# Kernel optimization log

Measured on AMD Instinct MI355X. Metric: run time of the kernel, lower is better.

Reference implementation:

```python
import jax, jax.numpy as jnp
import numpy as np
from jax import lax

C = 256        # shared head channels (out_ch)
NB = 6         # anchors per spatial location
NC = 9         # num_classes (incl. background)
B = 16         # batch
FM = [(38, 38), (19, 19), (10, 10), (5, 5), (3, 3), (1, 1)]
BIAS_PRIOR = -float(np.log((1.0 - 0.01) / 0.01))  # focal-style prior on cls bias


def _conv(x, w, b):
    # 3x3 conv, stride 1, SAME padding, NCHW/OIHW
    y = lax.conv_general_dilated(x, w, (1, 1), 'SAME',
                                 dimension_numbers=('NCHW', 'OIHW', 'NCHW'))
    return y + b[None, :, None, None]


def _head(x, ws, bs):
    for w, b in zip(ws[:-1], bs[:-1]):
        x = jax.nn.relu(_conv(x, w, b))
    return _conv(x, ws[-1], bs[-1])


def setup_inputs() -> dict:
    key = jax.random.key(0)
    ks = jax.random.split(key, 20)
    d = {}
    for i, (h, w) in enumerate(FM):
        d[f'feat{i}'] = jax.random.normal(ks[i], (B, C, h, w), dtype=jnp.float32)
    for i in range(4):
        d[f'rw{i}'] = 0.01 * jax.random.normal(ks[6 + i], (C, C, 3, 3), dtype=jnp.float32)
        d[f'rb{i}'] = jnp.zeros((C,), jnp.float32)
    d['rw4'] = 0.01 * jax.random.normal(ks[10], (NB * 4, C, 3, 3), dtype=jnp.float32)
    d['rb4'] = jnp.zeros((NB * 4,), jnp.float32)
    for i in range(4):
        d[f'cw{i}'] = 0.01 * jax.random.normal(ks[11 + i], (C, C, 3, 3), dtype=jnp.float32)
        d[f'cb{i}'] = jnp.zeros((C,), jnp.float32)
    d['cw4'] = 0.01 * jax.random.normal(ks[15], (NB * NC, C, 3, 3), dtype=jnp.float32)
    cb4 = jnp.zeros((NB * NC,), jnp.float32)
    d['cb4'] = cb4.at[:NB].set(BIAS_PRIOR)  # bias_per_class = n_boxes entries
    return d


def reference(feat0, feat1, feat2, feat3, feat4, feat5,
              rw0, rw1, rw2, rw3, rw4, rb0, rb1, rb2, rb3, rb4,
              cw0, cw1, cw2, cw3, cw4, cb0, cb1, cb2, cb3, cb4):
    feats = [feat0, feat1, feat2, feat3, feat4, feat5]
    rws = [rw0, rw1, rw2, rw3, rw4]
    rbs = [rb0, rb1, rb2, rb3, rb4]
    cws = [cw0, cw1, cw2, cw3, cw4]
    cbs = [cb0, cb1, cb2, cb3, cb4]
    locs, confs = [], []
    for x in feats:
        n = x.shape[0]
        locs.append(_head(x, rws, rbs).reshape(n, 4, -1))       # [N,4,NB*H*W]
        confs.append(_head(x, cws, cbs).reshape(n, NC, -1))     # [N,NC,NB*H*W]
    bbox_delta = jnp.concatenate(locs, axis=2)   # [N, 4, total_anchors]
    confidences = jnp.concatenate(confs, axis=2)  # [N, NC, total_anchors]
    return bbox_delta, confidences
```

## Files before the change

### kernel.cpp

```cpp
#include <hip/hip_runtime.h>
#include <hip/hip_bf16.h>

typedef __attribute__((ext_vector_type(8))) __bf16 bf16x8;
typedef __attribute__((ext_vector_type(4))) float f32x4;

__device__ __forceinline__ unsigned short f2bf(float f) {
    unsigned int u = __float_as_uint(f);
    u += 0x7fff + ((u >> 16) & 1);
    return (unsigned short)(u >> 16);
}

__device__ __forceinline__ void gload16(const void* g, void* l) {
    __builtin_amdgcn_global_load_lds(
        (const __attribute__((address_space(1))) void*)g,
        (__attribute__((address_space(3))) void*)l, 16, 0, 0);
}

#define ZOFFB (31040 * 512)

__device__ __forceinline__ void tile256(int rt, int& rb, int& dim, int& row0) {
    if (rt < 91)       { rb = 0;     dim = 38; row0 = rt * 256; }
    else if (rt < 114) { rb = 23104; dim = 19; row0 = (rt - 91) * 256; }
    else if (rt < 121) { rb = 28880; dim = 10; row0 = (rt - 114) * 256; }
    else if (rt < 123) { rb = 30480; dim = 5;  row0 = (rt - 121) * 256; }
    else if (rt < 124) { rb = 30880; dim = 3;  row0 = (rt - 123) * 256; }
    else               { rb = 31024; dim = 1;  row0 = 0; }
    row0 += rb;
}

__device__ __forceinline__ void tile128(int rt, int& rb, int& dim, int& row0, int& aoff) {
    if (rt < 181)      { rb = 0;     dim = 38; row0 = rt * 128;         aoff = 0;     }
    else if (rt < 227) { rb = 23104; dim = 19; row0 = (rt - 181) * 128; aoff = 8664;  }
    else if (rt < 240) { rb = 28880; dim = 10; row0 = (rt - 227) * 128; aoff = 10830; }
    else if (rt < 244) { rb = 30480; dim = 5;  row0 = (rt - 240) * 128; aoff = 11430; }
    else if (rt < 246) { rb = 30880; dim = 3;  row0 = (rt - 244) * 128; aoff = 11580; }
    else               { rb = 31024; dim = 1;  row0 = (rt - 246) * 128; aoff = 11634; }
    row0 += rb;
}

struct WT { const float* src[10]; };
__global__ void wtrans_all(WT wt, unsigned short* __restrict__ Wb, unsigned short* __restrict__ WF) {
    int idx = blockIdx.x * 256 + threadIdx.x;
    if (idx >= 5013504) return;
    const float* src;
    unsigned short* dst;
    int lo, Cout;
    if (idx < 4718592) {
        int slot = idx / 589824;
        lo = idx - slot * 589824;
        src = wt.src[slot];
        dst = Wb + (size_t)slot * 589824;
        Cout = 256;
    } else {
        int r = idx - 4718592;
        int slot = r / 147456;
        lo = r - slot * 147456;
        src = wt.src[8 + slot];
        dst = WF + (size_t)slot * 147456;
        Cout = slot ? 54 : 24;
    }
    int co = lo / 2304;
    int k  = lo - co * 2304;
    int tap = k >> 8;
    int ci  = k & 255;
    float v = (co < Cout) ? src[(co * 256 + ci) * 9 + tap] : 0.0f;
    dst[lo] = f2bf(v);
}

struct FT { const float* src[6]; };
__global__ void ftrans_all(FT ft, unsigned short* __restrict__ X0) {
    int idx = blockIdx.x * 256 + threadIdx.x;
    if (idx >= 993280) return;
    int row = idx >> 5;
    int c8  = (idx & 31) << 3;
    int m, rb, dim;
    if (row < 23104)      { m = 0; rb = 0;     dim = 38; }
    else if (row < 28880) { m = 1; rb = 23104; dim = 19; }
    else if (row < 30480) { m = 2; rb = 28880; dim = 10; }
    else if (row < 30880) { m = 3; rb = 30480; dim = 5;  }
    else if (row < 31024) { m = 4; rb = 30880; dim = 3;  }
    else                  { m = 5; rb = 31024; dim = 1;  }
    int HW = dim * dim;
    int rel = row - rb;
    int b = rel / HW;
    int hw = rel - b * HW;
    const float* s = ft.src[m] + (size_t)(b * 256 + c8) * HW + hw;
    union { unsigned short u[8]; uint4 v; } tmp;
#pragma unroll
    for (int j = 0; j < 8; ++j) tmp.u[j] = f2bf(s[(size_t)j * HW]);
    *reinterpret_cast<uint4*>(X0 + ((size_t)row << 8) + c8) = tmp.v;
}

struct GArgs {
    const unsigned short* X[2];
    const unsigned short* W[2];
    const float* B[2];
    unsigned short* Y[2];
};

__global__ __launch_bounds__(512, 2) void conv_gemm(GArgs ga) {
    __shared__ unsigned char As[65536];
    __shared__ unsigned char Bs[65536];

    const int hz = blockIdx.y;
    const unsigned char* __restrict__ Xb = (const unsigned char*)ga.X[hz];
    const unsigned char* __restrict__ Wt = (const unsigned char*)ga.W[hz];
    const float* __restrict__ bias = ga.B[hz];
    unsigned short* __restrict__ Y = ga.Y[hz];

    int rb, dim, row0;
    tile256(blockIdx.x, rb, dim, row0);
    const int HWm = dim * dim;
    const int rowEnd = rb + 16 * HWm;

    const int tid = threadIdx.x;
    const int lane = tid & 63, wid = tid >> 6;
    const int lr = lane & 15, lg = lane >> 4;
    const int wm = wid >> 2, wn = wid & 3;

    const int sr0 = tid >> 2;
    const int xsw = (((tid & 3) ^ ((sr0 >> 1) & 3)) << 4);
    const unsigned char* Zr = Xb + ZOFFB + xsw;

    int gg[2], ay[2], ax[2];
    bool av[2];
#pragma unroll
    for (int it = 0; it < 2; ++it) {
        int g = row0 + sr0 + it * 128;
        bool v = g < rowEnd;
        int rel = v ? (g - rb) : 0;
        int b = rel / HWm;
        int hw = rel - b * HWm;
        int y = hw / dim;
        gg[it] = g; ay[it] = y; ax[it] = hw - y * dim; av[it] = v;
    }

    const unsigned char* bsrc0 = Wt + (size_t)sr0 * 4608 + xsw;
    const unsigned char* bsrc1 = Wt + (size_t)(sr0 + 128) * 4608 + xsw;

    auto tapA = [&](int tap, const unsigned char*& p0, const unsigned char*& p1) {
        int q3 = tap / 3;
        int dy = q3 - 1, dx = tap - q3 * 3 - 1;
        int ddd = dy * dim + dx;
        bool v0 = av[0] && ((unsigned)(ay[0] + dy) < (unsigned)dim) && ((unsigned)(ax[0] + dx) < (unsigned)dim);
        bool v1 = av[1] && ((unsigned)(ay[1] + dy) < (unsigned)dim) && ((unsigned)(ax[1] + dx) < (unsigned)dim);
        p0 = v0 ? Xb + (size_t)(gg[0] + ddd) * 512 + xsw : Zr;
        p1 = v1 ? Xb + (size_t)(gg[1] + ddd) * 512 + xsw : Zr;
    };

    const int fswz = ((lg ^ ((lr >> 1) & 3)) << 4);
    const int aRd = (wm * 128 + lr) * 64 + fswz;
    const int bRd = (wn * 64 + lr) * 64 + fswz;
    const int dSt = wid * 1024;

    f32x4 acc[8][4];
#pragma unroll
    for (int i = 0; i < 8; ++i)
#pragma unroll
        for (int j = 0; j < 4; ++j) acc[i][j] = (f32x4){0.f, 0.f, 0.f, 0.f};

    const unsigned char *aC0, *aC1, *aN0, *aN1;
    tapA(0, aC0, aC1);
#pragma unroll
    for (int kt = 0; kt < 3; ++kt) {
        gload16(aC0 + kt * 64, As + kt * 16384 + dSt);
        gload16(aC1 + kt * 64, As + kt * 16384 + 8192 + dSt);
        gload16(bsrc0 + kt * 64, Bs + kt * 16384 + dSt);
        gload16(bsrc1 + kt * 64, Bs + kt * 16384 + 8192 + dSt);
    }

#pragma unroll 1
    for (int tap = 0; tap < 9; ++tap) {
        if (tap < 8) tapA(tap + 1, aN0, aN1);
        else { aN0 = Zr; aN1 = Zr; }
        const unsigned char* bT0 = bsrc0 + tap * 512;
        const unsigned char* bT1 = bsrc1 + tap * 512;

#pragma unroll
        for (int kc = 0; kc < 8; ++kc) {
            const int bufc = kc & 3;
            const int bufs = (kc + 3) & 3;

            asm volatile("s_waitcnt vmcnt(8)" ::: "memory");
            __builtin_amdgcn_s_barrier();

            {
                const unsigned char *sa0, *sa1;
                if (kc < 5) { sa0 = aC0 + (kc + 3) * 64; sa1 = aC1 + (kc + 3) * 64; }
                else        { sa0 = aN0 + (kc - 5) * 64; sa1 = aN1 + (kc - 5) * 64; }
                gload16(sa0, As + bufs * 16384 + dSt);
                gload16(sa1, As + bufs * 16384 + 8192 + dSt);
                gload16(bT0 + (kc + 3) * 64, Bs + bufs * 16384 + dSt);
                gload16(bT1 + (kc + 3) * 64, Bs + bufs * 16384 + 8192 + dSt);
            }

            bf16x8 a[4], b[4];
#pragma unroll
            for (int j = 0; j < 4; ++j)
                b[j] = *(const bf16x8*)(Bs + bufc * 16384 + bRd + j * 1024);
#pragma unroll
            for (int i = 0; i < 4; ++i)
                a[i] = *(const bf16x8*)(As + bufc * 16384 + aRd + i * 1024);
            asm volatile("s_waitcnt lgkmcnt(0)" ::: "memory");
            __builtin_amdgcn_sched_barrier(0);
            __builtin_amdgcn_s_setprio(1);
#pragma unroll
            for (int i = 0; i < 4; ++i)
#pragma unroll
                for (int j = 0; j < 4; ++j)
                    acc[i][j] = __builtin_amdgcn_mfma_f32_16x16x32_bf16(a[i], b[j], acc[i][j], 0, 0, 0);
            __builtin_amdgcn_s_setprio(0);

            bf16x8 a2[4];
#pragma unroll
            for (int i = 0; i < 4; ++i)
                a2[i] = *(const bf16x8*)(As + bufc * 16384 + aRd + (i + 4) * 1024);
            asm volatile("s_waitcnt lgkmcnt(0)" ::: "memory");
            __builtin_amdgcn_sched_barrier(0);
            __builtin_amdgcn_s_setprio(1);
#pragma unroll
            for (int i = 0; i < 4; ++i)
#pragma unroll
                for (int j = 0; j < 4; ++j)
                    acc[i + 4][j] = __builtin_amdgcn_mfma_f32_16x16x32_bf16(a2[i], b[j], acc[i + 4][j], 0, 0, 0);
            __builtin_amdgcn_s_setprio(0);
        }
        aC0 = aN0; aC1 = aN1;
    }

    float bj[4];
#pragma unroll
    for (int j = 0; j < 4; ++j) bj[j] = bias[wn * 64 + j * 16 + lr];
#pragma unroll
    for (int i = 0; i < 8; ++i) {
        int rbase = row0 + wm * 128 + i * 16 + lg * 4;
#pragma unroll
        for (int rr = 0; rr < 4; ++rr) {
            int orow = rbase + rr;
            if (orow < rowEnd) {
                size_t yb = (size_t)orow * 256 + wn * 64 + lr;
#pragma unroll
                for (int j = 0; j < 4; ++j) {
                    float v = acc[i][j][rr] + bj[j];
                    Y[yb + j * 16] = f2bf(fmaxf(v, 0.f));
                }
            }
        }
    }
}

struct FArgs {
    const unsigned short* X[2];
    const unsigned short* W[2];
    const float* B[2];
    float* out;
    int hbase;
};

__global__ __launch_bounds__(256) void conv_final(FArgs fa) {
    __shared__ unsigned char As[2][8192];
    __shared__ unsigned char Bs[2][4096];

    const int zi = blockIdx.z;
    const int hz = zi + fa.hbase;
    const unsigned char* Xb = (const unsigned char*)fa.X[zi];
    const unsigned char* Wt = (const unsigned char*)fa.W[zi];
    const float* bias = fa.B[zi];
    float* out = fa.out;

    int rb, dim, row0, aoff;
    tile128(blockIdx.x, rb, dim, row0, aoff);
    const int HWm = dim * dim;
    const int rowEnd = rb + 16 * HWm;

    const int tid = threadIdx.x;
    const int lane = tid & 63, wid = tid >> 6;
    const int lr = lane & 15, lg = lane >> 4;

    const int swz16 = (((lane & 3) ^ ((lane >> 3) & 3)) << 4);
    const int srow = wid * 16 + (lane >> 2);

    int ay[2], ax[2], arel[2];
    bool av0[2];
#pragma unroll
    for (int it = 0; it < 2; ++it) {
        int r = row0 + it * 64 + srow;
        bool v = r < rowEnd;
        int rel = v ? (r - rb) : 0;
        int b = rel / HWm;
        int hw = rel - b * HWm;
        int y = hw / dim;
        ay[it] = y; ax[it] = hw - y * dim; arel[it] = rel; av0[it] = v;
    }

    const unsigned char* bB = Wt + (size_t)srow * 4608 + swz16;

    const int fsw = ((lg ^ ((lr >> 1) & 3)) << 4);
    const int aRd = (wid * 32 + lr) * 64 + fsw;
    const int bRd = lr * 64 + fsw;
    const int dA0 = wid * 1024;

    f32x4 acc[2][4];
#pragma unroll
    for (int i = 0; i < 2; ++i)
#pragma unroll
        for (int j = 0; j < 4; ++j) acc[i][j] = (f32x4){0.f, 0.f, 0.f, 0.f};

    auto tapPtr = [&](int tap, const unsigned char** aP) {
        int q3 = tap / 3;
        int dy = q3 - 1, dx = tap - q3 * 3 - 1;
#pragma unroll
        for (int it = 0; it < 2; ++it) {
            bool v = av0[it] && ((unsigned)(ay[it] + dy) < (unsigned)dim)
                             && ((unsigned)(ax[it] + dx) < (unsigned)dim);
            int off = v ? (rb + arel[it] + dy * dim + dx) * 512 : ZOFFB;
            aP[it] = Xb + off + swz16;
        }
    };

    const unsigned char* aP[2];
    tapPtr(0, aP);
    gload16(aP[0], &As[0][dA0]);
    gload16(aP[1], &As[0][dA0 + 4096]);
    gload16(bB, &Bs[0][dA0]);
    __syncthreads();

#pragma unroll 1
    for (int tap = 0; tap < 9; ++tap) {
        const unsigned char* aPn[2];
        if (tap < 8) tapPtr(tap + 1, aPn);
        else { aPn[0] = aP[0]; aPn[1] = aP[1]; }
        const unsigned char* bP = bB + tap * 512;

#pragma unroll
        for (int kin = 0; kin < 8; ++kin) {
            const int cur = kin & 1, nxt = cur ^ 1;
            if (kin < 7) {
                gload16(aP[0] + (kin + 1) * 64, &As[nxt][dA0]);
                gload16(aP[1] + (kin + 1) * 64, &As[nxt][dA0 + 4096]);
                gload16(bP + (kin + 1) * 64, &Bs[nxt][dA0]);
            } else if (tap < 8) {
                gload16(aPn[0], &As[nxt][dA0]);
                gload16(aPn[1], &As[nxt][dA0 + 4096]);
                gload16(bP + 512, &Bs[nxt][dA0]);
            }
            bf16x8 af[2], bg[4];
#pragma unroll
            for (int i = 0; i < 2; ++i)
                af[i] = *(const bf16x8*)(&As[cur][0] + aRd + i * 1024);
#pragma unroll
            for (int j = 0; j < 4; ++j)
                bg[j] = *(const bf16x8*)(&Bs[cur][0] + bRd + j * 1024);
#pragma unroll
            for (int i = 0; i < 2; ++i)
#pragma unroll
                for (int j = 0; j < 4; ++j)
                    acc[i][j] = __builtin_amdgcn_mfma_f32_16x16x32_bf16(af[i], bg[j], acc[i][j], 0, 0, 0);
            __syncthreads();
        }
        aP[0] = aPn[0]; aP[1] = aPn[1];
    }

    const int Cout = hz ? 54 : 24;
#pragma unroll
    for (int i = 0; i < 2; ++i) {
        int rbase = row0 + wid * 32 + i * 16 + lg * 4;
#pragma unroll
        for (int r = 0; r < 4; ++r) {
            int orow = rbase + r;
            if (orow < rowEnd) {
                int rel = orow - rb;
                int b = rel / HWm;
                int hw = rel - b * HWm;
#pragma unroll
                for (int j = 0; j < 4; ++j) {
                    int oc = j * 16 + lr;
                    if (oc < Cout) {
                        int q = oc / 6;
                        int s = oc - q * 6;
                        int anchor = aoff + s * HWm + hw;
                        float v = acc[i][j][r] + bias[oc];
                        if (hz)
                            out[744960 + (size_t)b * 104760 + (size_t)q * 11640 + anchor] = v;
                        else
                            out[(size_t)b * 46560 + (size_t)q * 11640 + anchor] = v;
                    }
                }
            }
        }
    }
}

extern "C" void kernel_launch(void* const* d_in, const int* in_sizes, int n_in,
                              void* d_out, int out_size, void* d_ws, size_t ws_size,
                              hipStream_t stream) {
    (void)in_sizes; (void)n_in; (void)out_size;

    const float* rw[5]  = {(const float*)d_in[6],  (const float*)d_in[8],
                           (const float*)d_in[10], (const float*)d_in[12],
                           (const float*)d_in[14]};
    const float* rbv[5] = {(const float*)d_in[7],  (const float*)d_in[9],
                           (const float*)d_in[11], (const float*)d_in[13],
                           (const float*)d_in[15]};
    const float* cw[5]  = {(const float*)d_in[16], (const float*)d_in[18],
                           (const float*)d_in[20], (const float*)d_in[22],
                           (const float*)d_in[24]};
    const float* cbv[5] = {(const float*)d_in[17], (const float*)d_in[19],
                           (const float*)d_in[21], (const float*)d_in[23],
                           (const float*)d_in[25]};

    const size_t ACTB = 31041ull * 512;
    const size_t WMAT = 589824;
    const size_t WBYTES = 8 * WMAT * 2;
    const size_t WFBYTES = 2 * 147456 * 2;
    const size_t needF = 4 * ACTB + WBYTES + WFBYTES;
    const size_t needS = 3 * ACTB + WBYTES + WFBYTES;

    unsigned char* ws = (unsigned char*)d_ws;
    bool fused = (ws_size >= needF);
    if (!fused && ws_size < needS) return;

    int nact = fused ? 4 : 3;
    unsigned short* act[4];
    for (int i = 0; i < nact; ++i) act[i] = (unsigned short*)(ws + (size_t)i * ACTB);
    unsigned short* Wb = (unsigned short*)(ws + (size_t)nact * ACTB);
    unsigned short* WF = (unsigned short*)(ws + (size_t)nact * ACTB + WBYTES);

    for (int i = 0; i < nact; ++i)
        hipMemsetAsync((unsigned char*)act[i] + ZOFFB, 0, 512, stream);

    WT wt;
    for (int l = 0; l < 4; ++l) { wt.src[l] = rw[l]; wt.src[4 + l] = cw[l]; }
    wt.src[8] = rw[4]; wt.src[9] = cw[4];
    wtrans_all<<<19584, 256, 0, stream>>>(wt, Wb, WF);

    FT ft;
    for (int i = 0; i < 6; ++i) ft.src[i] = (const float*)d_in[i];
    ftrans_all<<<3880, 256, 0, stream>>>(ft, act[0]);

    const unsigned short* Wr[5], *Wc[5];
    for (int l = 0; l < 4; ++l) {
        Wr[l] = Wb + (size_t)l * WMAT;
        Wc[l] = Wb + (size_t)(4 + l) * WMAT;
    }
    Wr[4] = WF; Wc[4] = WF + 147456;

    if (fused) {
        unsigned short* X0 = act[0];
        unsigned short* P = act[1];
        unsigned short* Q = act[2];
        unsigned short* R = act[3];
        GArgs l1 = {{X0, X0}, {Wr[0], Wc[0]}, {rbv[0], cbv[0]}, {P, Q}};
        GArgs l2 = {{P,  Q},  {Wr[1], Wc[1]}, {rbv[1], cbv[1]}, {X0, R}};
        GArgs l3 = {{X0, R},  {Wr[2], Wc[2]}, {rbv[2], cbv[2]}, {P, Q}};
        GArgs l4 = {{P,  Q},  {Wr[3], Wc[3]}, {rbv[3], cbv[3]}, {X0, R}};
        conv_gemm<<<dim3(125, 2), 512, 0, stream>>>(l1);
        conv_gemm<<<dim3(125, 2), 512, 0, stream>>>(l2);
        conv_gemm<<<dim3(125, 2), 512, 0, stream>>>(l3);
        conv_gemm<<<dim3(125, 2), 512, 0, stream>>>(l4);
        FArgs lf = {{X0, R}, {Wr[4], Wc[4]}, {rbv[4], cbv[4]}, (float*)d_out, 0};
        conv_final<<<dim3(247, 1, 2), 256, 0, stream>>>(lf);
    } else {
        unsigned short* X0 = act[0];
        unsigned short* A1 = act[1];
        unsigned short* A2 = act[2];
        for (int h = 0; h < 2; ++h) {
            const unsigned short* const* W = h ? Wc : Wr;
            const float* const* bs = h ? cbv : rbv;
            GArgs l1 = {{X0, X0}, {W[0], W[0]}, {bs[0], bs[0]}, {A1, A1}};
            GArgs l2 = {{A1, A1}, {W[1], W[1]}, {bs[1], bs[1]}, {A2, A2}};
            GArgs l3 = {{A2, A2}, {W[2], W[2]}, {bs[2], bs[2]}, {A1, A1}};
            GArgs l4 = {{A1, A1}, {W[3], W[3]}, {bs[3], bs[3]}, {A2, A2}};
            conv_gemm<<<dim3(125, 1), 512, 0, stream>>>(l1);
            conv_gemm<<<dim3(125, 1), 512, 0, stream>>>(l2);
            conv_gemm<<<dim3(125, 1), 512, 0, stream>>>(l3);
            conv_gemm<<<dim3(125, 1), 512, 0, stream>>>(l4);
            FArgs lf = {{A2, A2}, {W[4], W[4]}, {bs[4], bs[4]}, (float*)d_out, h};
            conv_final<<<dim3(247, 1, 1), 256, 0, stream>>>(lf);
        }
    }
}
```

Baseline: 413.2 us.

## Register double-buffer LDS fragments in conv GEMM and fold halo zeroing into ftrans

The main GEMM loop now prefetches the next k-chunk's A and B fragments from LDS into a second register set while the MFMAs run on the current set. It also merges the two half-MFMA phases into a single 8x4 block and relaxes the waits (vmcnt 4, lgkmcnt 12). Separately, the per-buffer zero-halo memsets are replaced by extra threads in the feature-transpose kernel, removing several small API calls. Holding two register fragment sets raises VGPR pressure, which could hurt occupancy or cause spills.

```diff
diff --git a/kernel.cpp b/kernel.cpp
--- a/kernel.cpp
+++ b/kernel.cpp
@@ -67,10 +67,15 @@
     dst[lo] = f2bf(v);
 }
 
-struct FT { const float* src[6]; };
+struct FT { const float* src[6]; unsigned short* halo[4]; int nh; };
 __global__ void ftrans_all(FT ft, unsigned short* __restrict__ X0) {
     int idx = blockIdx.x * 256 + threadIdx.x;
-    if (idx >= 993280) return;
+    if (idx >= 993280) {
+        int idx2 = idx - 993280;
+        int buf = idx2 >> 8, off = idx2 & 255;
+        if (buf < ft.nh) ft.halo[buf][off] = 0;
+        return;
+    }
     int row = idx >> 5;
     int c8  = (idx & 31) << 3;
     int m, rb, dim;
@@ -159,6 +164,8 @@
 #pragma unroll
         for (int j = 0; j < 4; ++j) acc[i][j] = (f32x4){0.f, 0.f, 0.f, 0.f};
 
+    bf16x8 rA[2][8], rB[2][4];
+
     const unsigned char *aC0, *aC1, *aN0, *aN1;
     tapA(0, aC0, aC1);
 #pragma unroll
@@ -168,6 +175,12 @@
         gload16(bsrc0 + kt * 64, Bs + kt * 16384 + dSt);
         gload16(bsrc1 + kt * 64, Bs + kt * 16384 + 8192 + dSt);
     }
+    asm volatile("s_waitcnt vmcnt(8)" ::: "memory");
+    __builtin_amdgcn_s_barrier();
+#pragma unroll
+    for (int i = 0; i < 8; ++i) rA[0][i] = *(const bf16x8*)(As + aRd + i * 1024);
+#pragma unroll
+    for (int j = 0; j < 4; ++j) rB[0][j] = *(const bf16x8*)(Bs + bRd + j * 1024);
 
 #pragma unroll 1
     for (int tap = 0; tap < 9; ++tap) {
@@ -178,51 +191,38 @@
 
 #pragma unroll
         for (int kc = 0; kc < 8; ++kc) {
-            const int bufc = kc & 3;
-            const int bufs = (kc + 3) & 3;
-
-            asm volatile("s_waitcnt vmcnt(8)" ::: "memory");
+            const int cur = kc & 1;
+            const int nslot = (kc + 1) & 3;
+            const int sslot = (kc + 3) & 3;
+
+            asm volatile("s_waitcnt vmcnt(4)" ::: "memory");
             __builtin_amdgcn_s_barrier();
 
             {
                 const unsigned char *sa0, *sa1;
                 if (kc < 5) { sa0 = aC0 + (kc + 3) * 64; sa1 = aC1 + (kc + 3) * 64; }
                 else        { sa0 = aN0 + (kc - 5) * 64; sa1 = aN1 + (kc - 5) * 64; }
-                gload16(sa0, As + bufs * 16384 + dSt);
-                gload16(sa1, As + bufs * 16384 + 8192 + dSt);
-                gload16(bT0 + (kc + 3) * 64, Bs + bufs * 16384 + dSt);
-                gload16(bT1 + (kc + 3) * 64, Bs + bufs * 16384 + 8192 + dSt);
+                gload16(sa0, As + sslot * 16384 + dSt);
+                gload16(sa1, As + sslot * 16384 + 8192 + dSt);
+                gload16(bT0 + (kc + 3) * 64, Bs + sslot * 16384 + dSt);
+                gload16(bT1 + (kc + 3) * 64, Bs + sslot * 16384 + 8192 + dSt);
             }
 
-            bf16x8 a[4], b[4];
+#pragma unroll
+            for (int i = 0; i < 8; ++i)
+                rA[cur ^ 1][i] = *(const bf16x8*)(As + nslot * 16384 + aRd + i * 1024);
 #pragma unroll
             for (int j = 0; j < 4; ++j)
-                b[j] = *(const bf16x8*)(Bs + bufc * 16384 + bRd + j * 1024);
-#pragma unroll
-            for (int i = 0; i < 4; ++i)
-                a[i] = *(const bf16x8*)(As + bufc * 16384 + aRd + i * 1024);
-            asm volatile("s_waitcnt lgkmcnt(0)" ::: "memory");
+                rB[cur ^ 1][j] = *(const bf16x8*)(Bs + nslot * 16384 + bRd + j * 1024);
+
+            asm volatile("s_waitcnt lgkmcnt(12)" ::: "memory");
             __builtin_amdgcn_sched_barrier(0);
             __builtin_amdgcn_s_setprio(1);
 #pragma unroll
-            for (int i = 0; i < 4; ++i)
+            for (int i = 0; i < 8; ++i)
 #pragma unroll
                 for (int j = 0; j < 4; ++j)
-                    acc[i][j] = __builtin_amdgcn_mfma_f32_16x16x32_bf16(a[i], b[j], acc[i][j], 0, 0, 0);
-            __builtin_amdgcn_s_setprio(0);
-
-            bf16x8 a2[4];
-#pragma unroll
-            for (int i = 0; i < 4; ++i)
-                a2[i] = *(const bf16x8*)(As + bufc * 16384 + aRd + (i + 4) * 1024);
-            asm volatile("s_waitcnt lgkmcnt(0)" ::: "memory");
-            __builtin_amdgcn_sched_barrier(0);
-            __builtin_amdgcn_s_setprio(1);
-#pragma unroll
-            for (int i = 0; i < 4; ++i)
-#pragma unroll
-                for (int j = 0; j < 4; ++j)
-                    acc[i + 4][j] = __builtin_amdgcn_mfma_f32_16x16x32_bf16(a2[i], b[j], acc[i + 4][j], 0, 0, 0);
+                    acc[i][j] = __builtin_amdgcn_mfma_f32_16x16x32_bf16(rA[cur][i], rB[cur][j], acc[i][j], 0, 0, 0);
             __builtin_amdgcn_s_setprio(0);
         }
         aC0 = aN0; aC1 = aN1;
@@ -426,9 +426,6 @@
     unsigned short* Wb = (unsigned short*)(ws + (size_t)nact * ACTB);
     unsigned short* WF = (unsigned short*)(ws + (size_t)nact * ACTB + WBYTES);
 
-    for (int i = 0; i < nact; ++i)
-        hipMemsetAsync((unsigned char*)act[i] + ZOFFB, 0, 512, stream);
-
     WT wt;
     for (int l = 0; l < 4; ++l) { wt.src[l] = rw[l]; wt.src[4 + l] = cw[l]; }
     wt.src[8] = rw[4]; wt.src[9] = cw[4];
@@ -436,7 +433,10 @@
 
     FT ft;
     for (int i = 0; i < 6; ++i) ft.src[i] = (const float*)d_in[i];
-    ftrans_all<<<3880, 256, 0, stream>>>(ft, act[0]);
+    for (int i = 0; i < 4; ++i)
+        ft.halo[i] = (unsigned short*)((unsigned char*)act[i < nact ? i : 0] + ZOFFB);
+    ft.nh = nact;
+    ftrans_all<<<3884, 256, 0, stream>>>(ft, act[0]);
 
     const unsigned short* Wr[5], *Wc[5];
     for (int l = 0; l < 4; ++l) {
```

Result: no change. 418.0 us (+1.2%).

## Split A/B tile prefetch across half-steps and fold halo memsets into feature transpose

Applied to the files above, without the earlier changes.

The GEMM main loop now reads LDS fragments before issuing the next A prefetch, and issues the B prefetch between the two MFMA half-blocks. Extra barriers are added so each buffer is reused safely. The goal is to spread global-to-LDS traffic over the iteration and overlap it with MFMA work. The separate hipMemsetAsync calls that zero the halo rows are removed, and the feature transpose kernel gets four extra blocks that zero them instead, cutting launch overhead. The added barriers (four per k-chunk instead of one) may cost more synchronization than the finer overlap saves.

```diff
diff --git a/kernel.cpp b/kernel.cpp
--- a/kernel.cpp
+++ b/kernel.cpp
@@ -67,10 +67,15 @@
     dst[lo] = f2bf(v);
 }
 
-struct FT { const float* src[6]; };
+struct FT { const float* src[6]; unsigned short* halo[4]; int nh; };
 __global__ void ftrans_all(FT ft, unsigned short* __restrict__ X0) {
     int idx = blockIdx.x * 256 + threadIdx.x;
-    if (idx >= 993280) return;
+    if (idx >= 993280) {
+        int idx2 = idx - 993280;
+        int buf = idx2 >> 8, off = idx2 & 255;
+        if (buf < ft.nh) ft.halo[buf][off] = 0;
+        return;
+    }
     int row = idx >> 5;
     int c8  = (idx & 31) << 3;
     int m, rb, dim;
@@ -168,6 +173,8 @@
         gload16(bsrc0 + kt * 64, Bs + kt * 16384 + dSt);
         gload16(bsrc1 + kt * 64, Bs + kt * 16384 + 8192 + dSt);
     }
+    asm volatile("s_waitcnt vmcnt(8)" ::: "memory");
+    __builtin_amdgcn_s_barrier();
 
 #pragma unroll 1
     for (int tap = 0; tap < 9; ++tap) {
@@ -175,32 +182,29 @@
         else { aN0 = Zr; aN1 = Zr; }
         const unsigned char* bT0 = bsrc0 + tap * 512;
         const unsigned char* bT1 = bsrc1 + tap * 512;
+        const unsigned char* bN0 = bT0 + 512;
+        const unsigned char* bN1 = bT1 + 512;
 
 #pragma unroll
         for (int kc = 0; kc < 8; ++kc) {
             const int bufc = kc & 3;
             const int bufs = (kc + 3) & 3;
-
-            asm volatile("s_waitcnt vmcnt(8)" ::: "memory");
-            __builtin_amdgcn_s_barrier();
-
+            const unsigned char* ab = As + bufc * 16384;
+            const unsigned char* bb = Bs + bufc * 16384;
+
+            bf16x8 rB[4], rA[4];
+#pragma unroll
+            for (int j = 0; j < 4; ++j) rB[j] = *(const bf16x8*)(bb + bRd + j * 1024);
+#pragma unroll
+            for (int i = 0; i < 4; ++i) rA[i] = *(const bf16x8*)(ab + aRd + i * 1024);
             {
                 const unsigned char *sa0, *sa1;
                 if (kc < 5) { sa0 = aC0 + (kc + 3) * 64; sa1 = aC1 + (kc + 3) * 64; }
                 else        { sa0 = aN0 + (kc - 5) * 64; sa1 = aN1 + (kc - 5) * 64; }
                 gload16(sa0, As + bufs * 16384 + dSt);
                 gload16(sa1, As + bufs * 16384 + 8192 + dSt);
-                gload16(bT0 + (kc + 3) * 64, Bs + bufs * 16384 + dSt);
-                gload16(bT1 + (kc + 3) * 64, Bs + bufs * 16384 + 8192 + dSt);
             }
-
-            bf16x8 a[4], b[4];
-#pragma unroll
-            for (int j = 0; j < 4; ++j)
-                b[j] = *(const bf16x8*)(Bs + bufc * 16384 + bRd + j * 1024);
-#pragma unroll
-            for (int i = 0; i < 4; ++i)
-                a[i] = *(const bf16x8*)(As + bufc * 16384 + aRd + i * 1024);
+            __builtin_amdgcn_s_barrier();
             asm volatile("s_waitcnt lgkmcnt(0)" ::: "memory");
             __builtin_amdgcn_sched_barrier(0);
             __builtin_amdgcn_s_setprio(1);
@@ -208,13 +212,22 @@
             for (int i = 0; i < 4; ++i)
 #pragma unroll
                 for (int j = 0; j < 4; ++j)
-                    acc[i][j] = __builtin_amdgcn_mfma_f32_16x16x32_bf16(a[i], b[j], acc[i][j], 0, 0, 0);
+                    acc[i][j] = __builtin_amdgcn_mfma_f32_16x16x32_bf16(rA[i], rB[j], acc[i][j], 0, 0, 0);
             __builtin_amdgcn_s_setprio(0);
-
-            bf16x8 a2[4];
-#pragma unroll
-            for (int i = 0; i < 4; ++i)
-                a2[i] = *(const bf16x8*)(As + bufc * 16384 + aRd + (i + 4) * 1024);
+            __builtin_amdgcn_s_barrier();
+
+            bf16x8 rA2[4];
+#pragma unroll
+            for (int i = 0; i < 4; ++i) rA2[i] = *(const bf16x8*)(ab + aRd + (i + 4) * 1024);
+            {
+                const unsigned char *sb0, *sb1;
+                if (kc < 5) { sb0 = bT0 + (kc + 3) * 64; sb1 = bT1 + (kc + 3) * 64; }
+                else        { sb0 = bN0 + (kc - 5) * 64; sb1 = bN1 + (kc - 5) * 64; }
+                gload16(sb0, Bs + bufs * 16384 + dSt);
+                gload16(sb1, Bs + bufs * 16384 + 8192 + dSt);
+            }
+            asm volatile("s_waitcnt vmcnt(8)" ::: "memory");
+            __builtin_amdgcn_s_barrier();
             asm volatile("s_waitcnt lgkmcnt(0)" ::: "memory");
             __builtin_amdgcn_sched_barrier(0);
             __builtin_amdgcn_s_setprio(1);
@@ -222,8 +235,9 @@
             for (int i = 0; i < 4; ++i)
 #pragma unroll
                 for (int j = 0; j < 4; ++j)
-                    acc[i + 4][j] = __builtin_amdgcn_mfma_f32_16x16x32_bf16(a2[i], b[j], acc[i + 4][j], 0, 0, 0);
+                    acc[i + 4][j] = __builtin_amdgcn_mfma_f32_16x16x32_bf16(rA2[i], rB[j], acc[i + 4][j], 0, 0, 0);
             __builtin_amdgcn_s_setprio(0);
+            __builtin_amdgcn_s_barrier();
         }
         aC0 = aN0; aC1 = aN1;
     }
@@ -426,9 +440,6 @@
     unsigned short* Wb = (unsigned short*)(ws + (size_t)nact * ACTB);
     unsigned short* WF = (unsigned short*)(ws + (size_t)nact * ACTB + WBYTES);
 
-    for (int i = 0; i < nact; ++i)
-        hipMemsetAsync((unsigned char*)act[i] + ZOFFB, 0, 512, stream);
-
     WT wt;
     for (int l = 0; l < 4; ++l) { wt.src[l] = rw[l]; wt.src[4 + l] = cw[l]; }
     wt.src[8] = rw[4]; wt.src[9] = cw[4];
@@ -436,7 +447,10 @@
 
     FT ft;
     for (int i = 0; i < 6; ++i) ft.src[i] = (const float*)d_in[i];
-    ftrans_all<<<3880, 256, 0, stream>>>(ft, act[0]);
+    for (int i = 0; i < 4; ++i)
+        ft.halo[i] = (unsigned short*)((unsigned char*)act[i < nact ? i : 0] + ZOFFB);
+    ft.nh = nact;
+    ftrans_all<<<3884, 256, 0, stream>>>(ft, act[0]);
 
     const unsigned short* Wr[5], *Wc[5];
     for (int l = 0; l < 4; ++l) {
```

Result: faster. 404.9 us (-2.0%).
